# Performance work log

Measured on AMD Instinct MI355X. Metric: run time of the kernel, lower is better.

The kernel has to match this reference:

```python
import math
import jax, jax.numpy as jnp
import numpy as np

SAMPLE_RATIO = 0.25
K_NN = 5


def grid_index(loc_orig, H, W):
    # loc in [-1,1] -> nearest grid cell index (row-major)
    loc = jnp.clip(loc_orig, -1.0, 1.0) * 0.5 + 0.5
    ix = jnp.clip(jnp.round(loc[..., 0] * (W - 1)).astype(jnp.int32), 0, W - 1)
    iy = jnp.clip(jnp.round(loc[..., 1] * (H - 1)).astype(jnp.int32), 0, H - 1)
    return iy * W + ix  # [B, N0]


def token2map(x, loc_orig, idx_agg, H, W):
    # scatter token features (replicated to original points) into HxW grid, cell-average
    B, N, C = x.shape
    N0 = idx_agg.shape[1]
    idx_hw = grid_index(loc_orig, H, W)
    off = jnp.arange(B, dtype=jnp.int32)[:, None]
    idx_hw_flat = (idx_hw + off * (H * W)).reshape(-1)
    value = jnp.ones((B * N0,), x.dtype)
    all_w = jax.ops.segment_sum(value, idx_hw_flat, num_segments=B * H * W) + 1e-6
    value = value / all_w[idx_hw_flat]
    x_src = jnp.take_along_axis(x, idx_agg[..., None], axis=1).reshape(B * N0, C)
    x_map = jax.ops.segment_sum(x_src * value[:, None], idx_hw_flat, num_segments=B * H * W)
    return x_map.reshape(B, H, W, C).transpose(0, 3, 1, 2)  # [B,C,H,W]


def map2token(x_map, N, loc_orig, idx_agg, agg_weight):
    # gather grid features back to tokens, weighted by per-token-normalized agg_weight
    B, C, H, W = x_map.shape
    N0 = idx_agg.shape[1]
    idx_hw = grid_index(loc_orig, H, W)
    off = jnp.arange(B, dtype=jnp.int32)[:, None]
    idx_tok_flat = (idx_agg + off * N).reshape(-1)
    idx_hw_flat = (idx_hw + off * (H * W)).reshape(-1)
    value = agg_weight.reshape(-1).astype(x_map.dtype)
    all_w = jax.ops.segment_sum(value, idx_tok_flat, num_segments=B * N) + 1e-6
    value = value / all_w[idx_tok_flat]
    feat = x_map.transpose(0, 2, 3, 1).reshape(B * H * W, C)[idx_hw_flat]
    out = jax.ops.segment_sum(feat * value[:, None], idx_tok_flat, num_segments=B * N)
    return out.reshape(B, N, C)


def cluster_dpc_knn(x, Ns, k):
    # DPC-KNN clustering (no_grad in original -> stop_gradient)
    B, N, C = x.shape
    x = jax.lax.stop_gradient(x)
    x2 = jnp.sum(x * x, axis=-1)
    d2 = x2[:, :, None] + x2[:, None, :] - 2.0 * jnp.einsum('bic,bjc->bij', x, x)
    dist = jnp.sqrt(jnp.maximum(d2, 0.0)) / jnp.sqrt(jnp.asarray(C, x.dtype))
    dist_nearest = -jax.lax.top_k(-dist, k)[0]                 # k smallest dists (incl self)
    density = jnp.exp(-jnp.mean(dist_nearest ** 2, axis=-1))    # [B,N]
    # deterministic tiny tie-break noise (original uses torch.rand*1e-6)
    density = density + jax.random.uniform(jax.random.key(42), density.shape, density.dtype) * 1e-6
    mask = (density[:, None, :] > density[:, :, None]).astype(x.dtype)
    dist_max = jnp.max(dist.reshape(B, -1), axis=-1)[:, None, None]
    dist_ind = jnp.min(dist * mask + dist_max * (1.0 - mask), axis=-1)
    score = dist_ind * density
    index_down = jax.lax.top_k(score, Ns)[1]                    # [B,Ns] cluster centers
    dist_c = jnp.take_along_axis(dist, index_down[:, :, None], axis=1)  # [B,Ns,N]
    idx_cluster = jnp.argmin(dist_c, axis=1).astype(jnp.int32)  # [B,N]
    # centers belong to their own cluster
    flat = (index_down + jnp.arange(B)[:, None] * N).reshape(-1)
    own = jnp.tile(jnp.arange(Ns, dtype=jnp.int32), B)
    idx_cluster = idx_cluster.reshape(-1).at[flat].set(own).reshape(B, N)
    return idx_cluster


def merge_tokens(x, idx_cluster, Ns, weight, idx_agg):
    # weighted average of tokens per cluster; propagate mapping/weights to original points
    B, N, C = x.shape
    idx = (idx_cluster + jnp.arange(B, dtype=jnp.int32)[:, None] * Ns).reshape(-1)
    w = weight.reshape(-1)
    all_w = jax.ops.segment_sum(w, idx, num_segments=B * Ns) + 1e-6
    nw = w / all_w[idx]
    x_merged = jax.ops.segment_sum(x.reshape(B * N, C) * nw[:, None], idx,
                                   num_segments=B * Ns).reshape(B, Ns, C)
    norm_weight = nw.reshape(B, N, 1)
    idx_agg_new = jnp.take_along_axis(idx_cluster, idx_agg, axis=1)          # [B,N0]
    weight_t = jnp.take_along_axis(norm_weight, idx_agg[..., None], axis=1)  # [B,N0,1]
    return x_merged, idx_agg_new, weight_t


def ctm_forward(x, loc_orig, idx_agg, agg_weight, conv_w, conv_b, skip_w, ln_g, ln_b,
                conf_w, conf_b, H, W):
    B, N, C = x.shape
    x_map = token2map(x, loc_orig, idx_agg, H, W)
    x_map = jax.lax.conv_general_dilated(
        x_map, conv_w, window_strides=(2, 2), padding=((1, 1), (1, 1)),
        dimension_numbers=('NCHW', 'OIHW', 'NCHW')) + conv_b[None, :, None, None]
    xt = map2token(x_map, N, loc_orig, idx_agg, agg_weight) + x @ skip_w.T
    mu = jnp.mean(xt, axis=-1, keepdims=True)
    var = jnp.mean((xt - mu) ** 2, axis=-1, keepdims=True)
    xt = (xt - mu) / jnp.sqrt(var + 1e-5) * ln_g + ln_b
    conf = xt @ conf_w.T + conf_b          # [B,N,1]
    weight = jnp.exp(conf)
    Ns = max(math.ceil(N * SAMPLE_RATIO), 1)
    idx_cluster = cluster_dpc_knn(xt, Ns, K_NN)
    x_down, idx_agg_down, weight_t = merge_tokens(xt, idx_cluster, Ns, weight, idx_agg)
    agg_weight_down = agg_weight * weight_t
    agg_weight_down = agg_weight_down / jnp.max(agg_weight_down, axis=1, keepdims=True)
    # down_block is identity in this reference
    return x_down, idx_agg_down, agg_weight_down


def setup_inputs() -> dict:
    key = jax.random.key(0)
    ks = jax.random.split(key, 10)
    B, N, C, C2, H, W = 4, 3136, 64, 128, 56, 56
    return {
        'x': jax.random.normal(ks[0], (B, N, C), jnp.float32),
        'loc_orig': jax.random.normal(ks[1], (B, N, 2), jnp.float32),
        'idx_agg': jax.random.randint(ks[2], (B, N), 0, N),
        'agg_weight': jax.random.uniform(ks[3], (B, N, 1), jnp.float32, 0.1, 1.0),
        'conv_w': jax.random.normal(ks[4], (C2, C, 3, 3), jnp.float32) * 0.02,
        'conv_b': jnp.zeros((C2,), jnp.float32),
        'skip_w': jax.random.normal(ks[5], (C2, C), jnp.float32) * 0.02,
        'ln_g': jnp.ones((C2,), jnp.float32),
        'ln_b': jnp.zeros((C2,), jnp.float32),
        'conf_w': jax.random.normal(ks[6], (1, C2), jnp.float32) * 0.02,
        'conf_b': jnp.zeros((1,), jnp.float32),
        'H': 56,
        'W': 56,
    }


def reference(x, loc_orig, idx_agg, agg_weight, conv_w, conv_b, skip_w, ln_g, ln_b,
              conf_w, conf_b, H, W):
    return ctm_forward(x, loc_orig, idx_agg, agg_weight, conv_w, conv_b, skip_w,
                       ln_g, ln_b, conf_w, conf_b, H, W)
```

## Files before the change

### kernel.cpp

```cpp
#include <hip/hip_runtime.h>
#include <math.h>
#include <float.h>

#define Bq   4
#define Nq   3136
#define Cq   64
#define C2q  128
#define Hq   56
#define Wq   56
#define HWq  (Hq*Wq)
#define HOq  28
#define WOq  28
#define HWOq (HOq*WOq)
#define NSq  784
#define KNN  5
#define BNq  (Bq*Nq)

#define T64   64
#define KC    32
#define NIT64 (Nq/T64)
#define NT_C  ((NSq+T64-1)/T64)
#define NSPL  8
#define NSPA  2
#define LDP   34

__device__ __constant__ int c_spl[NSPL + 1]  = {0, 7, 13, 19, 25, 31, 37, 43, 49};
__device__ __constant__ int c_spla[NSPA + 1] = {0, 7, 13};

typedef unsigned int   u32;
typedef unsigned long long u64;
typedef __attribute__((ext_vector_type(4))) double d64x4;

static __device__ __forceinline__ void atomicMaxPosD(double* p, double v) {
    atomicMax((u64*)p, (u64)__double_as_longlong(v));
}
static __device__ __forceinline__ int clampTok(int t) {
    return min(max(t, 0), Nq - 1);
}

static __device__ __forceinline__ void ins5(double* a, double v) {
    if (v < a[KNN - 1]) {
        a[KNN - 1] = v;
        #pragma unroll
        for (int m = KNN - 1; m > 0; m--)
            if (a[m] < a[m - 1]) { double t = a[m]; a[m] = a[m - 1]; a[m - 1] = t; }
    }
}
static __device__ __forceinline__ void cex(double& a, double& b) {
    double lo = fmin(a, b), hi = fmax(a, b); a = lo; b = hi;
}
static __device__ __forceinline__ void merge5(double* a, const double* p) {
    double t0 = fmin(a[0], p[4]);
    double t1 = fmin(a[1], p[3]);
    double t2 = fmin(a[2], p[2]);
    double t3 = fmin(a[3], p[1]);
    double t4 = fmin(a[4], p[0]);
    cex(t0, t1); cex(t1, t2); cex(t2, t3); cex(t3, t4);
    cex(t0, t1); cex(t1, t2); cex(t2, t3);
    cex(t0, t1); cex(t1, t2);
    cex(t0, t1);
    a[0] = t0; a[1] = t1; a[2] = t2; a[3] = t3; a[4] = t4;
}

static __device__ __forceinline__ int mfma_mode_probe(int l4, int l15) {
    d64x4 p;
    #pragma unroll
    for (int v = 0; v < 4; v++) p[v] = 0.0;
    double a1 = (l4 == 0) ? (double)(16 * l15) : 0.0;
    double b1 = (l4 == 0) ? 1.0 : 0.0;
    p = __builtin_amdgcn_mfma_f64_16x16x4f64(a1, b1, p, 0, 0, 0);
    double a2 = (l4 == 0) ? 1.0 : 0.0;
    double b2 = (l4 == 0) ? (double)l15 : 0.0;
    p = __builtin_amdgcn_mfma_f64_16x16x4f64(a2, b2, p, 0, 0, 0);
    bool ok0 = true, ok1 = true;
    #pragma unroll
    for (int v = 0; v < 4; v++) {
        ok0 = ok0 && (p[v] == (double)(16 * (4 * l4 + v) + l15));
        ok1 = ok1 && (p[v] == (double)(16 * (l4 + 4 * v) + l15));
    }
    return __all(ok0) ? 0 : (__all(ok1) ? 1 : 2);
}

static __device__ __forceinline__ u32 rotl32(u32 x, int d) { return (x << d) | (x >> (32 - d)); }
static __device__ __forceinline__ float tf_uniform(int t) {
    const u32 k0 = 0u, k1 = 42u;
    const u32 ks2 = k0 ^ k1 ^ 0x1BD11BDAu;
    u32 ks[3] = { k0, k1, ks2 };
    bool lo = (t < 6272);
    u32 cx0 = lo ? (u32)t : (u32)(t - 6272);
    u32 cx1 = lo ? (u32)(t + 6272) : (u32)t;
    u32 x0 = cx0 + ks[0];
    u32 x1 = cx1 + ks[1];
    const int R0[4] = {13, 15, 26, 6};
    const int R1[4] = {17, 29, 16, 24};
    #pragma unroll
    for (int i = 0; i < 5; i++) {
        const int* rot = (i % 2 == 0) ? R0 : R1;
        #pragma unroll
        for (int r = 0; r < 4; r++) { x0 += x1; x1 = rotl32(x1, rot[r]); x1 ^= x0; }
        x0 += ks[(i + 1) % 3];
        x1 += ks[(i + 2) % 3] + (u32)(i + 1);
    }
    u32 bits = lo ? x0 : x1;
    u32 fb = (bits >> 9) | 0x3f800000u;
    float f; __builtin_memcpy(&f, &fb, 4);
    return f - 1.0f;
}

static __device__ __forceinline__ int gridIndex(float lx, float ly, int Wd, int Hd) {
    double x = fmin(fmax((double)lx, -1.0), 1.0) * 0.5 + 0.5;
    double y = fmin(fmax((double)ly, -1.0), 1.0) * 0.5 + 0.5;
    int ix = (int)rint(x * (double)(Wd - 1)); ix = min(max(ix, 0), Wd - 1);
    int iy = (int)rint(y * (double)(Hd - 1)); iy = min(max(iy, 0), Hd - 1);
    return iy * Wd + ix;
}

__global__ void ctm_fallback(float* out, int n) {
    int t = blockIdx.x * blockDim.x + threadIdx.x;
    if (t < n) out[t] = 0.0f;
}

__global__ void ctm_prep(const float* __restrict__ loc, const int* __restrict__ idx_agg,
                         const float* __restrict__ aggw,
                         int* cell56, int* cell28, int* cnt56, double* allwtok) {
    int t = blockIdx.x * blockDim.x + threadIdx.x;
    if (t >= BNq) return;
    int b = t / Nq;
    float lx = loc[2 * t], ly = loc[2 * t + 1];
    int c56 = gridIndex(lx, ly, Wq, Hq);
    int c28 = gridIndex(lx, ly, WOq, HOq);
    cell56[t] = c56; cell28[t] = c28;
    atomicAdd(&cnt56[b * HWq + c56], 1);
    int tok = clampTok(idx_agg[t]);
    atomicAdd(&allwtok[b * Nq + tok], (double)aggw[t]);
}

__global__ void ctm_t2m(const float* __restrict__ x, const int* __restrict__ idx_agg,
                        const int* __restrict__ cell56, const int* __restrict__ cnt56,
                        double* xmap56T) {
    int id = blockIdx.x * blockDim.x + threadIdx.x;
    if (id >= BNq * Cq) return;
    int t = id / Cq, c = id - t * Cq;
    int b = t / Nq;
    int cell = cell56[t];
    double v = 1.0 / ((double)cnt56[b * HWq + cell] + 1e-6);
    double xv = (double)x[(size_t)(b * Nq + clampTok(idx_agg[t])) * Cq + c];
    atomicAdd(&xmap56T[((size_t)b * HWq + cell) * Cq + c], xv * v);
}

__global__ void ctm_wt(const float* __restrict__ w, float* wT) {
    int id = blockIdx.x * blockDim.x + threadIdx.x;
    if (id >= C2q * Cq * 9) return;
    int co = id & (C2q - 1);
    int rem = id >> 7;
    int tap = rem % 9;
    int ci = rem / 9;
    wT[id] = w[(size_t)co * Cq * 9 + ci * 9 + tap];
}

__global__ __launch_bounds__(256)
void ctm_conv(const double* __restrict__ xmap56T, const float* __restrict__ wT,
              const float* __restrict__ bias, double* xmap28T) {
    __shared__ double sIn[2][9][Cq];
    int blk = blockIdx.x;
    int b  = blk & (Bq - 1);
    int cp = blk >> 2;
    int tid = threadIdx.x;
    int co = tid & (C2q - 1);
    int cl = tid >> 7;
    const double* xb = xmap56T + (size_t)b * HWq * Cq;
    for (int idx = tid; idx < 2 * 9 * Cq; idx += 256) {
        int cell_l = idx / (9 * Cq);
        int rem = idx - cell_l * (9 * Cq);
        int tap = rem >> 6;
        int ci  = rem & 63;
        int cell = 2 * cp + cell_l;
        int ox = cell % WOq, oy = cell / WOq;
        int ky = tap / 3, kx = tap - ky * 3;
        int iy = 2 * oy + ky - 1, ix = 2 * ox + kx - 1;
        double v = 0.0;
        if (iy >= 0 && iy < Hq && ix >= 0 && ix < Wq)
            v = xb[(size_t)(iy * Wq + ix) * Cq + ci];
        sIn[cell_l][tap][ci] = v;
    }
    __syncthreads();
    double acc = (double)bias[co];
    for (int ci = 0; ci < Cq; ci++) {
        #pragma unroll
        for (int tap = 0; tap < 9; tap++)
            acc += sIn[cl][tap][ci] * (double)wT[(size_t)(ci * 9 + tap) * C2q + co];
    }
    int cell = 2 * cp + cl;
    xmap28T[((size_t)b * HWOq + cell) * C2q + co] = acc;
}

__global__ void ctm_m2t(const double* __restrict__ xmap28T, const float* __restrict__ aggw,
                        const int* __restrict__ idx_agg, const int* __restrict__ cell28,
                        const double* __restrict__ allwtok, double* xt) {
    int id = blockIdx.x * blockDim.x + threadIdx.x;
    if (id >= BNq * C2q) return;
    int t = id / C2q, c = id - t * C2q;
    int b = t / Nq;
    int tok = clampTok(idx_agg[t]);
    double v = (double)aggw[t] / (allwtok[b * Nq + tok] + 1e-6);
    double f = xmap28T[((size_t)b * HWOq + cell28[t]) * C2q + c];
    atomicAdd(&xt[(size_t)(b * Nq + tok) * C2q + c], f * v);
}

__global__ __launch_bounds__(C2q)
void ctm_finalize(double* xt, const float* __restrict__ x, const float* __restrict__ skipw,
                  const float* __restrict__ lng, const float* __restrict__ lnb,
                  const float* __restrict__ confw, const float* __restrict__ confb,
                  double* x2o, double* weightv) {
    int bn = blockIdx.x; int c = threadIdx.x;
    int lane = c & 63, w = c >> 6;
    double* row = xt + (size_t)bn * C2q;
    const float* xr = x + (size_t)bn * Cq;
    double acc = row[c];
    const float* sw = skipw + c * Cq;
    #pragma unroll 16
    for (int k = 0; k < Cq; k++) acc += (double)xr[k] * (double)sw[k];
    __shared__ double slot[4][2];
    double s = acc;
    #pragma unroll
    for (int m = 1; m <= 32; m <<= 1) s += __shfl_xor(s, m);
    if (lane == 0) slot[0][w] = s;
    __syncthreads();
    double mu = (slot[0][0] + slot[0][1]) * (1.0 / C2q);
    double d = acc - mu;
    s = d * d;
    #pragma unroll
    for (int m = 1; m <= 32; m <<= 1) s += __shfl_xor(s, m);
    if (lane == 0) slot[1][w] = s;
    __syncthreads();
    double var = (slot[1][0] + slot[1][1]) * (1.0 / C2q);
    double v = d / sqrt(var + 1e-5) * (double)lng[c] + (double)lnb[c];
    row[c] = v;
    s = v * v;
    #pragma unroll
    for (int m = 1; m <= 32; m <<= 1) s += __shfl_xor(s, m);
    if (lane == 0) slot[2][w] = s;
    double s2 = v * (double)confw[c];
    #pragma unroll
    for (int m = 1; m <= 32; m <<= 1) s2 += __shfl_xor(s2, m);
    if (lane == 0) slot[3][w] = s2;
    __syncthreads();
    if (c == 0) {
        x2o[bn] = slot[2][0] + slot[2][1];
        weightv[bn] = exp(slot[3][0] + slot[3][1] + (double)confb[0]);
    }
}


__global__ __launch_bounds__(256, 2)
void ctm_pass1(const double* __restrict__ xt, const double* __restrict__ x2,
               double* pbest, double* pmax, double* d2buf, int dostore) {
    __shared__ double sBB[2][T64][LDP];
    __shared__ double sx2j[2][T64];
    int blk = blockIdx.x;
    int b  = blk & (Bq - 1);
    int s  = (blk >> 2) & (NSPL - 1);
    int it = blk >> 5;
    int tid = threadIdx.x;
    const double* xtb = xt + (size_t)b * Nq * C2q;
    const double* x2b = x2 + (size_t)b * Nq;
    int i0 = it * T64;
    int jt_beg = c_spl[s], jt_end = c_spl[s + 1];

    int wv = tid >> 6, ln = tid & 63;
    int l15 = ln & 15, l4 = ln >> 4;
    int mode = mfma_mode_probe(l4, l15);

    if (mode < 2) {
        int rw[4];
        #pragma unroll
        for (int v = 0; v < 4; v++) rw[v] = (mode == 0) ? (4 * l4 + v) : (l4 + 4 * v);
        int rbase = i0 + wv * 16;
        double a_reg[4][8];
        const double* arow = xtb + (size_t)(i0 + wv * 16 + l15) * C2q + l4;
        #pragma unroll
        for (int kc = 0; kc < 4; kc++)
            #pragma unroll
            for (int st = 0; st < 8; st++)
                a_reg[kc][st] = arow[kc * KC + 4 * st];
        double x2i[4];
        #pragma unroll
        for (int v = 0; v < 4; v++) x2i[v] = x2b[rbase + rw[v]];
        double best[4][KNN]; double mx[4];
        #pragma unroll
        for (int v = 0; v < 4; v++) {
            mx[v] = -DBL_MAX;
            #pragma unroll
            for (int k = 0; k < KNN; k++) best[v][k] = DBL_MAX;
        }
        {
            int j0 = jt_beg * T64;
            #pragma unroll
            for (int w = 0; w < 4; w++) {
                int idx = tid + w * 256; int r = idx >> 4, c = (idx & 15) * 2;
                *(double2*)&sBB[0][r][c] = *(const double2*)&xtb[(size_t)(j0 + r) * C2q + c];
            }
            if (tid < T64) sx2j[0][tid] = x2b[j0 + tid];
        }
        __syncthreads();
        int q = 0;
        for (int jt = jt_beg; jt < jt_end; jt++) {
            int j0 = jt * T64;
            d64x4 acc[4];
            #pragma unroll
            for (int bc = 0; bc < 4; bc++)
                #pragma unroll
                for (int v = 0; v < 4; v++) acc[bc][v] = 0.0;
            #pragma unroll
            for (int kc = 0; kc < 4; kc++) {
                const int cb = kc & 1, nb = cb ^ 1, nkc = (kc + 1) & 3;
                const bool lastk = (kc == 3);
                bool hn = !lastk || (jt + 1 < jt_end);
                int nj0 = lastk ? j0 + T64 : j0;
                double2 sreg[4]; double xr = 0.0;
                if (hn) {
                    #pragma unroll
                    for (int w = 0; w < 4; w++) {
                        int idx = tid + w * 256; int r = idx >> 4, c = (idx & 15) * 2;
                        sreg[w] = *(const double2*)&xtb[(size_t)(nj0 + r) * C2q + nkc * KC + c];
                    }
                    if (lastk && tid < T64) xr = x2b[nj0 + tid];
                }
                #pragma unroll
                for (int st = 0; st < 8; st++) {
                    double av = a_reg[kc][st];
                    #pragma unroll
                    for (int bc = 0; bc < 4; bc++) {
                        double bv = sBB[cb][bc * 16 + l15][4 * st + l4];
                        acc[bc] = __builtin_amdgcn_mfma_f64_16x16x4f64(av, bv, acc[bc], 0, 0, 0);
                    }
                }
                if (hn) {
                    #pragma unroll
                    for (int w = 0; w < 4; w++) {
                        int idx = tid + w * 256; int r = idx >> 4, c = (idx & 15) * 2;
                        *(double2*)&sBB[nb][r][c] = sreg[w];
                    }
                    if (lastk && tid < T64) sx2j[q ^ 1][tid] = xr;
                }
                __syncthreads();
            }
            #pragma unroll
            for (int bc = 0; bc < 4; bc++) {
                double xj = sx2j[q][bc * 16 + l15];
                #pragma unroll
                for (int v = 0; v < 4; v++) {
                    double d2 = x2i[v] + xj - 2.0 * acc[bc][v];
                    if (dostore)
                        d2buf[(size_t)(b * Nq + rbase + rw[v]) * Nq + (j0 + bc * 16 + l15)] = d2;
                    mx[v] = fmax(mx[v], d2);
                    ins5(best[v], d2);
                }
            }
            q ^= 1;
        }
        for (int m = 1; m <= 8; m <<= 1) {
            #pragma unroll
            for (int v = 0; v < 4; v++) {
                double p[KNN];
                #pragma unroll
                for (int k = 0; k < KNN; k++) p[k] = __shfl_xor(best[v][k], m);
                mx[v] = fmax(mx[v], __shfl_xor(mx[v], m));
                merge5(best[v], p);
            }
        }
        if (l15 == 0) {
            #pragma unroll
            for (int v = 0; v < 4; v++) {
                int gi = b * Nq + rbase + rw[v];
                size_t base = ((size_t)s * BNq + gi) * KNN;
                #pragma unroll
                for (int k = 0; k < KNN; k++) pbest[base + k] = best[v][k];
                pmax[(size_t)s * BNq + gi] = mx[v];
            }
        }
    } else {
        double (*sA)[LDP] = sBB[0];
        double (*sB)[LDP] = sBB[1];
        int tx = tid & 15, ty = tid >> 4;
        double x2i[4];
        #pragma unroll
        for (int r = 0; r < 4; r++) x2i[r] = x2b[i0 + ty + 16 * r];
        double best[4][KNN]; double mx[4];
        #pragma unroll
        for (int r = 0; r < 4; r++) {
            mx[r] = -DBL_MAX;
            #pragma unroll
            for (int k = 0; k < KNN; k++) best[r][k] = DBL_MAX;
        }
        for (int jt = jt_beg; jt < jt_end; jt++) {
            int j0 = jt * T64;
            double acc[4][4];
            #pragma unroll
            for (int r = 0; r < 4; r++)
                #pragma unroll
                for (int q = 0; q < 4; q++) acc[r][q] = 0.0;
            for (int kc = 0; kc < 4; kc++) {
                __syncthreads();
                #pragma unroll
                for (int idx = tid; idx < T64 * KC / 2; idx += 256) {
                    int r = idx >> 4, c = (idx & 15) * 2;
                    *(double2*)&sA[r][c] = *(const double2*)&xtb[(size_t)(i0 + r) * C2q + kc * KC + c];
                    *(double2*)&sB[r][c] = *(const double2*)&xtb[(size_t)(j0 + r) * C2q + kc * KC + c];
                }
                if (kc == 0 && tid < T64) sx2j[0][tid] = x2b[j0 + tid];
                __syncthreads();
                #pragma unroll 4
                for (int cc = 0; cc < KC; cc += 2) {
                    double2 xi[4], xj[4];
                    #pragma unroll
                    for (int r = 0; r < 4; r++) xi[r] = *(const double2*)&sA[ty + 16 * r][cc];
                    #pragma unroll
                    for (int q = 0; q < 4; q++) xj[q] = *(const double2*)&sB[tx + 16 * q][cc];
                    #pragma unroll
                    for (int r = 0; r < 4; r++)
                        #pragma unroll
                        for (int q = 0; q < 4; q++) acc[r][q] += xi[r].x * xj[q].x;
                    #pragma unroll
                    for (int r = 0; r < 4; r++)
                        #pragma unroll
                        for (int q = 0; q < 4; q++) acc[r][q] += xi[r].y * xj[q].y;
                }
            }
            #pragma unroll
            for (int r = 0; r < 4; r++)
                #pragma unroll
                for (int q = 0; q < 4; q++) {
                    double d2 = x2i[r] + sx2j[0][tx + 16 * q] - 2.0 * acc[r][q];
                    if (dostore)
                        d2buf[(size_t)(b * Nq + i0 + ty + 16 * r) * Nq + (j0 + tx + 16 * q)] = d2;
                    mx[r] = fmax(mx[r], d2);
                    ins5(best[r], d2);
                }
        }
        for (int m = 1; m <= 8; m <<= 1) {
            #pragma unroll
            for (int r = 0; r < 4; r++) {
                double p[KNN];
                #pragma unroll
                for (int k = 0; k < KNN; k++) p[k] = __shfl_xor(best[r][k], m);
                mx[r] = fmax(mx[r], __shfl_xor(mx[r], m));
                merge5(best[r], p);
            }
        }
        if (tx == 0) {
            #pragma unroll
            for (int r = 0; r < 4; r++) {
                int gi = b * Nq + i0 + ty + 16 * r;
                size_t base = ((size_t)s * BNq + gi) * KNN;
                #pragma unroll
                for (int k = 0; k < KNN; k++) pbest[base + k] = best[r][k];
                pmax[(size_t)s * BNq + gi] = mx[r];
            }
        }
    }
}

__global__ void ctm_merge1(const double* __restrict__ pbest, const double* __restrict__ pmax,
                           double* density, double* maxd2) {
    int t = blockIdx.x * blockDim.x + threadIdx.x;
    if (t >= BNq) return;
    double a[KNN];
    #pragma unroll
    for (int k = 0; k < KNN; k++) a[k] = pbest[(size_t)t * KNN + k];
    double mxv = pmax[t];
    #pragma unroll
    for (int s = 1; s < NSPL; s++) {
        double p[KNN];
        #pragma unroll
        for (int k = 0; k < KNN; k++) p[k] = pbest[((size_t)s * BNq + t) * KNN + k];
        merge5(a, p);
        mxv = fmax(mxv, pmax[(size_t)s * BNq + t]);
    }
    double sum = 0.0;
    #pragma unroll
    for (int k = 0; k < KNN; k++) sum += fmax(a[k], 0.0);
    density[t] = exp(-sum / (double)(C2q * KNN)) + (double)(tf_uniform(t) * 1e-6f);
    atomicMaxPosD(&maxd2[t / Nq], mxv);
}

__global__ __launch_bounds__(256)
void ctm_pass2s(const double* __restrict__ d2buf, const double* __restrict__ density,
                double* pmin2) {
    int gid = blockIdx.x * 4 + (threadIdx.x >> 6);
    int lane = threadIdx.x & 63;
    if (gid >= BNq) return;
    int b = gid / Nq;
    int i = gid - b * Nq;
    const double* dr = d2buf + (size_t)gid * Nq;
    const double* db = density + (size_t)b * Nq;
    double di = db[i];
    double mn = DBL_MAX;
    for (int j = lane; j < Nq; j += 64) {
        double d2 = dr[j];
        if (db[j] > di) mn = fmin(mn, d2);
    }
    #pragma unroll
    for (int m = 1; m <= 32; m <<= 1) mn = fmin(mn, __shfl_xor(mn, m));
    if (lane == 0) pmin2[gid] = mn;
}

__global__ void ctm_merge2s(const double* __restrict__ pmin2, const double* __restrict__ maxd2,
                            const double* __restrict__ density, double* score) {
    int t = blockIdx.x * blockDim.x + threadIdx.x;
    if (t >= BNq) return;
    int b = t / Nq;
    double mm = fmin(maxd2[b], pmin2[t]);
    score[t] = sqrt(fmax(mm, 0.0)) / sqrt((double)C2q) * density[t];
}

__global__ __launch_bounds__(256, 2)
void ctm_pass2(const double* __restrict__ xt, const double* __restrict__ x2,
               const double* __restrict__ density, double* pmin) {
    __shared__ double sBB[2][T64][LDP];
    __shared__ double sx2j[2][T64];
    __shared__ double sdj[2][T64];
    int blk = blockIdx.x;
    int b  = blk & (Bq - 1);
    int s  = (blk >> 2) & (NSPL - 1);
    int it = blk >> 5;
    int tid = threadIdx.x;
    const double* xtb = xt + (size_t)b * Nq * C2q;
    const double* x2b = x2 + (size_t)b * Nq;
    const double* db  = density + (size_t)b * Nq;
    int i0 = it * T64;
    int jt_beg = c_spl[s], jt_end = c_spl[s + 1];

    int wv = tid >> 6, ln = tid & 63;
    int l15 = ln & 15, l4 = ln >> 4;
    int mode = mfma_mode_probe(l4, l15);

    if (mode < 2) {
        int rw[4];
        #pragma unroll
        for (int v = 0; v < 4; v++) rw[v] = (mode == 0) ? (4 * l4 + v) : (l4 + 4 * v);
        int rbase = i0 + wv * 16;
        double a_reg[4][8];
        const double* arow = xtb + (size_t)(i0 + wv * 16 + l15) * C2q + l4;
        #pragma unroll
        for (int kc = 0; kc < 4; kc++)
            #pragma unroll
            for (int st = 0; st < 8; st++)
                a_reg[kc][st] = arow[kc * KC + 4 * st];
        double x2i[4], di[4], mn[4];
        #pragma unroll
        for (int v = 0; v < 4; v++) {
            x2i[v] = x2b[rbase + rw[v]];
            di[v]  = db[rbase + rw[v]];
            mn[v]  = DBL_MAX;
        }
        {
            int j0 = jt_beg * T64;
            #pragma unroll
            for (int w = 0; w < 4; w++) {
                int idx = tid + w * 256; int r = idx >> 4, c = (idx & 15) * 2;
                *(double2*)&sBB[0][r][c] = *(const double2*)&xtb[(size_t)(j0 + r) * C2q + c];
            }
            if (tid < T64) { sx2j[0][tid] = x2b[j0 + tid]; sdj[0][tid] = db[j0 + tid]; }
        }
        __syncthreads();
        int q = 0;
        for (int jt = jt_beg; jt < jt_end; jt++) {
            int j0 = jt * T64;
            d64x4 acc[4];
            #pragma unroll
            for (int bc = 0; bc < 4; bc++)
                #pragma unroll
                for (int v = 0; v < 4; v++) acc[bc][v] = 0.0;
            #pragma unroll
            for (int kc = 0; kc < 4; kc++) {
                const int cb = kc & 1, nb = cb ^ 1, nkc = (kc + 1) & 3;
                const bool lastk = (kc == 3);
                bool hn = !lastk || (jt + 1 < jt_end);
                int nj0 = lastk ? j0 + T64 : j0;
                double2 sreg[4]; double xr = 0.0, dr = 0.0;
                if (hn) {
                    #pragma unroll
                    for (int w = 0; w < 4; w++) {
                        int idx = tid + w * 256; int r = idx >> 4, c = (idx & 15) * 2;
                        sreg[w] = *(const double2*)&xtb[(size_t)(nj0 + r) * C2q + nkc * KC + c];
                    }
                    if (lastk && tid < T64) { xr = x2b[nj0 + tid]; dr = db[nj0 + tid]; }
                }
                #pragma unroll
                for (int st = 0; st < 8; st++) {
                    double av = a_reg[kc][st];
                    #pragma unroll
                    for (int bc = 0; bc < 4; bc++) {
                        double bv = sBB[cb][bc * 16 + l15][4 * st + l4];
                        acc[bc] = __builtin_amdgcn_mfma_f64_16x16x4f64(av, bv, acc[bc], 0, 0, 0);
                    }
                }
                if (hn) {
                    #pragma unroll
                    for (int w = 0; w < 4; w++) {
                        int idx = tid + w * 256; int r = idx >> 4, c = (idx & 15) * 2;
                        *(double2*)&sBB[nb][r][c] = sreg[w];
                    }
                    if (lastk && tid < T64) { sx2j[q ^ 1][tid] = xr; sdj[q ^ 1][tid] = dr; }
                }
                __syncthreads();
            }
            #pragma unroll
            for (int bc = 0; bc < 4; bc++) {
                double xj = sx2j[q][bc * 16 + l15];
                double dj = sdj[q][bc * 16 + l15];
                #pragma unroll
                for (int v = 0; v < 4; v++) {
                    double d2 = x2i[v] + xj - 2.0 * acc[bc][v];
                    if (dj > di[v]) mn[v] = fmin(mn[v], d2);
                }
            }
            q ^= 1;
        }
        for (int m = 1; m <= 8; m <<= 1) {
            #pragma unroll
            for (int v = 0; v < 4; v++) mn[v] = fmin(mn[v], __shfl_xor(mn[v], m));
        }
        if (l15 == 0) {
            #pragma unroll
            for (int v = 0; v < 4; v++) {
                int gi = b * Nq + rbase + rw[v];
                pmin[(size_t)s * BNq + gi] = mn[v];
            }
        }
    } else {
        double (*sA)[LDP] = sBB[0];
        double (*sB)[LDP] = sBB[1];
        int tx = tid & 15, ty = tid >> 4;
        double x2i[4], di[4], mn[4];
        #pragma unroll
        for (int r = 0; r < 4; r++) {
            x2i[r] = x2b[i0 + ty + 16 * r];
            di[r]  = db[i0 + ty + 16 * r];
            mn[r]  = DBL_MAX;
        }
        for (int jt = jt_beg; jt < jt_end; jt++) {
            int j0 = jt * T64;
            double acc[4][4];
            #pragma unroll
            for (int r = 0; r < 4; r++)
                #pragma unroll
                for (int q = 0; q < 4; q++) acc[r][q] = 0.0;
            for (int kc = 0; kc < 4; kc++) {
                __syncthreads();
                #pragma unroll
                for (int idx = tid; idx < T64 * KC / 2; idx += 256) {
                    int r = idx >> 4, c = (idx & 15) * 2;
                    *(double2*)&sA[r][c] = *(const double2*)&xtb[(size_t)(i0 + r) * C2q + kc * KC + c];
                    *(double2*)&sB[r][c] = *(const double2*)&xtb[(size_t)(j0 + r) * C2q + kc * KC + c];
                }
                if (kc == 0 && tid < T64) { sx2j[0][tid] = x2b[j0 + tid]; sdj[0][tid] = db[j0 + tid]; }
                __syncthreads();
                #pragma unroll 4
                for (int cc = 0; cc < KC; cc += 2) {
                    double2 xi[4], xj[4];
                    #pragma unroll
                    for (int r = 0; r < 4; r++) xi[r] = *(const double2*)&sA[ty + 16 * r][cc];
                    #pragma unroll
                    for (int q = 0; q < 4; q++) xj[q] = *(const double2*)&sB[tx + 16 * q][cc];
                    #pragma unroll
                    for (int r = 0; r < 4; r++)
                        #pragma unroll
                        for (int q = 0; q < 4; q++) acc[r][q] += xi[r].x * xj[q].x;
                    #pragma unroll
                    for (int r = 0; r < 4; r++)
                        #pragma unroll
                        for (int q = 0; q < 4; q++) acc[r][q] += xi[r].y * xj[q].y;
                }
            }
            #pragma unroll
            for (int r = 0; r < 4; r++)
                #pragma unroll
                for (int q = 0; q < 4; q++) {
                    double d2 = x2i[r] + sx2j[0][tx + 16 * q] - 2.0 * acc[r][q];
                    if (sdj[0][tx + 16 * q] > di[r]) mn[r] = fmin(mn[r], d2);
                }
        }
        for (int m = 1; m <= 8; m <<= 1) {
            #pragma unroll
            for (int r = 0; r < 4; r++) mn[r] = fmin(mn[r], __shfl_xor(mn[r], m));
        }
        if (tx == 0) {
            #pragma unroll
            for (int r = 0; r < 4; r++) {
                int gi = b * Nq + i0 + ty + 16 * r;
                pmin[(size_t)s * BNq + gi] = mn[r];
            }
        }
    }
}

__global__ void ctm_merge2(const double* __restrict__ pmin, const double* __restrict__ maxd2,
                           const double* __restrict__ density, double* score) {
    int t = blockIdx.x * blockDim.x + threadIdx.x;
    if (t >= BNq) return;
    int b = t / Nq;
    double m = pmin[t];
    #pragma unroll
    for (int s = 1; s < NSPL; s++) m = fmin(m, pmin[(size_t)s * BNq + t]);
    double mm = fmin(maxd2[b], m);
    score[t] = sqrt(fmax(mm, 0.0)) / sqrt((double)C2q) * density[t];
}

__global__ __launch_bounds__(1024)
void ctm_sort(const double* __restrict__ score, int* index_down) {
    __shared__ double s[4096];
    __shared__ int   si[4096];
    int b = blockIdx.x, tid = threadIdx.x;
    for (int i = tid; i < 4096; i += 1024) {
        if (i < Nq) {
            double v = score[b * Nq + i];
            s[i] = isnan(v) ? -DBL_MAX : v;
            si[i] = i;
        } else { s[i] = -DBL_MAX; si[i] = 0x7fffffff; }
    }
    __syncthreads();
    for (int k = 2; k <= 4096; k <<= 1) {
        for (int j = k >> 1; j > 0; j >>= 1) {
            for (int i = tid; i < 4096; i += 1024) {
                int ixj = i ^ j;
                if (ixj > i) {
                    double s1 = s[i], s2 = s[ixj];
                    int i1 = si[i], i2 = si[ixj];
                    bool before_ij = (s1 > s2) || (s1 == s2 && i1 < i2);
                    bool before_ji = (s2 > s1) || (s2 == s1 && i2 < i1);
                    bool doswap = ((i & k) == 0) ? before_ji : before_ij;
                    if (doswap) { s[i] = s2; s[ixj] = s1; si[i] = i2; si[ixj] = i1; }
                }
            }
            __syncthreads();
        }
    }
    for (int t = tid; t < NSq; t += 1024) {
        int v = si[t];
        index_down[b * NSq + t] = ((unsigned)v < (unsigned)Nq) ? v : 0;
    }
}

__global__ __launch_bounds__(256, 2)
void ctm_assign(const double* __restrict__ xt, const double* __restrict__ x2,
                const int* __restrict__ index_down, double* pbd, int* pbs) {
    __shared__ double sBB[2][T64][LDP];
    __shared__ double sx2c[T64];
    __shared__ int    sidx[T64];
    int blk = blockIdx.x;
    int b  = blk & (Bq - 1);
    int s  = (blk >> 2) & (NSPA - 1);
    int it = blk >> 3;
    int tid = threadIdx.x;
    const double* xtb = xt + (size_t)b * Nq * C2q;
    const double* x2b = x2 + (size_t)b * Nq;
    int i0 = it * T64;
    int jt_beg = c_spla[s], jt_end = c_spla[s + 1];

    int wv = tid >> 6, ln = tid & 63;
    int l15 = ln & 15, l4 = ln >> 4;
    int mode = mfma_mode_probe(l4, l15);

    if (mode < 2) {
        int rw[4];
        #pragma unroll
        for (int v = 0; v < 4; v++) rw[v] = (mode == 0) ? (4 * l4 + v) : (l4 + 4 * v);
        int rbase = i0 + wv * 16;
        double a_reg[4][8];
        const double* arow = xtb + (size_t)(i0 + wv * 16 + l15) * C2q + l4;
        #pragma unroll
        for (int kc = 0; kc < 4; kc++)
            #pragma unroll
            for (int st = 0; st < 8; st++)
                a_reg[kc][st] = arow[kc * KC + 4 * st];
        double x2i[4], bd[4];
        int bs[4];
        #pragma unroll
        for (int v = 0; v < 4; v++) { x2i[v] = x2b[rbase + rw[v]]; bd[v] = DBL_MAX; bs[v] = NSq - 1; }
        for (int jt = jt_beg; jt < jt_end; jt++) {
            int j0 = jt * T64;
            __syncthreads();
            if (tid < T64) {
                int j = index_down[b * NSq + min(j0 + tid, NSq - 1)];
                sidx[tid] = j;
                sx2c[tid] = x2b[j];
            }
            __syncthreads();
            d64x4 acc[4];
            #pragma unroll
            for (int bc = 0; bc < 4; bc++)
                #pragma unroll
                for (int v = 0; v < 4; v++) acc[bc][v] = 0.0;
            for (int kc = 0; kc < 4; kc++) {
                if (kc) __syncthreads();
                #pragma unroll
                for (int idx = tid; idx < T64 * KC / 2; idx += 256) {
                    int r = idx >> 4, c = (idx & 15) * 2;
                    *(double2*)&sBB[0][r][c] = *(const double2*)&xtb[(size_t)sidx[r] * C2q + kc * KC + c];
                }
                __syncthreads();
                #pragma unroll
                for (int st = 0; st < 8; st++) {
                    double av = a_reg[kc][st];
                    #pragma unroll
                    for (int bc = 0; bc < 4; bc++) {
                        double bv = sBB[0][bc * 16 + l15][4 * st + l4];
                        acc[bc] = __builtin_amdgcn_mfma_f64_16x16x4f64(av, bv, acc[bc], 0, 0, 0);
                    }
                }
            }
            #pragma unroll
            for (int bc = 0; bc < 4; bc++) {
                int sc = j0 + bc * 16 + l15;
                double xc = sx2c[bc * 16 + l15];
                #pragma unroll
                for (int v = 0; v < 4; v++) {
                    double d = fmax(x2i[v] + xc - 2.0 * acc[bc][v], 0.0);
                    if (sc < NSq && (d < bd[v] || (d == bd[v] && sc < bs[v]))) { bd[v] = d; bs[v] = sc; }
                }
            }
        }
        for (int m = 1; m <= 8; m <<= 1) {
            #pragma unroll
            for (int v = 0; v < 4; v++) {
                double pd = __shfl_xor(bd[v], m);
                int    ps = __shfl_xor(bs[v], m);
                if (pd < bd[v] || (pd == bd[v] && ps < bs[v])) { bd[v] = pd; bs[v] = ps; }
            }
        }
        if (l15 == 0) {
            #pragma unroll
            for (int v = 0; v < 4; v++) {
                int gi = b * Nq + rbase + rw[v];
                pbd[(size_t)s * BNq + gi] = bd[v];
                pbs[(size_t)s * BNq + gi] = bs[v];
            }
        }
    } else {
        double (*sA)[LDP] = sBB[0];
        double (*sB)[LDP] = sBB[1];
        int tx = tid & 15, ty = tid >> 4;
        double x2i[4], bd[4];
        int bs[4];
        #pragma unroll
        for (int r = 0; r < 4; r++) { x2i[r] = x2b[i0 + ty + 16 * r]; bd[r] = DBL_MAX; bs[r] = NSq - 1; }
        for (int jt = jt_beg; jt < jt_end; jt++) {
            int j0 = jt * T64;
            __syncthreads();
            if (tid < T64) {
                int j = index_down[b * NSq + min(j0 + tid, NSq - 1)];
                sidx[tid] = j;
                sx2c[tid] = x2b[j];
            }
            __syncthreads();
            double acc[4][4];
            #pragma unroll
            for (int r = 0; r < 4; r++)
                #pragma unroll
                for (int q = 0; q < 4; q++) acc[r][q] = 0.0;
            for (int kc = 0; kc < 4; kc++) {
                if (kc) __syncthreads();
                #pragma unroll
                for (int idx = tid; idx < T64 * KC / 2; idx += 256) {
                    int r = idx >> 4, c = (idx & 15) * 2;
                    *(double2*)&sA[r][c] = *(const double2*)&xtb[(size_t)(i0 + r) * C2q + kc * KC + c];
                    *(double2*)&sB[r][c] = *(const double2*)&xtb[(size_t)sidx[r] * C2q + kc * KC + c];
                }
                __syncthreads();
                #pragma unroll 4
                for (int cc = 0; cc < KC; cc += 2) {
                    double2 xi[4], xj[4];
                    #pragma unroll
                    for (int r = 0; r < 4; r++) xi[r] = *(const double2*)&sA[ty + 16 * r][cc];
                    #pragma unroll
                    for (int q = 0; q < 4; q++) xj[q] = *(const double2*)&sB[tx + 16 * q][cc];
                    #pragma unroll
                    for (int r = 0; r < 4; r++)
                        #pragma unroll
                        for (int q = 0; q < 4; q++) acc[r][q] += xi[r].x * xj[q].x;
                    #pragma unroll
                    for (int r = 0; r < 4; r++)
                        #pragma unroll
                        for (int q = 0; q < 4; q++) acc[r][q] += xi[r].y * xj[q].y;
                }
            }
            #pragma unroll
            for (int r = 0; r < 4; r++)
                #pragma unroll
                for (int q = 0; q < 4; q++) {
                    int sc = j0 + tx + 16 * q;
                    double d = fmax(x2i[r] + sx2c[tx + 16 * q] - 2.0 * acc[r][q], 0.0);
                    if (sc < NSq && (d < bd[r] || (d == bd[r] && sc < bs[r]))) { bd[r] = d; bs[r] = sc; }
                }
        }
        for (int m = 1; m <= 8; m <<= 1) {
            #pragma unroll
            for (int r = 0; r < 4; r++) {
                double pd = __shfl_xor(bd[r], m);
                int    ps = __shfl_xor(bs[r], m);
                if (pd < bd[r] || (pd == bd[r] && ps < bs[r])) { bd[r] = pd; bs[r] = ps; }
            }
        }
        if (tx == 0) {
            #pragma unroll
            for (int r = 0; r < 4; r++) {
                int gi = b * Nq + i0 + ty + 16 * r;
                pbd[(size_t)s * BNq + gi] = bd[r];
                pbs[(size_t)s * BNq + gi] = bs[r];
            }
        }
    }
}

__global__ void ctm_merge3(const double* __restrict__ pbd, const int* __restrict__ pbs,
                           int* idx_cluster) {
    int t = blockIdx.x * blockDim.x + threadIdx.x;
    if (t >= BNq) return;
    double d0 = pbd[t];          int s0 = pbs[t];
    double d1 = pbd[BNq + t];    int s1 = pbs[BNq + t];
    bool take1 = (d1 < d0) || (d1 == d0 && s1 < s0);
    idx_cluster[t] = take1 ? s1 : s0;
}

__global__ void ctm_override(const int* __restrict__ index_down, int* idx_cluster) {
    int t = blockIdx.x * blockDim.x + threadIdx.x;
    if (t >= Bq * NSq) return;
    int b = t / NSq, sc = t - b * NSq;
    int j = index_down[t];
    if ((unsigned)j < (unsigned)Nq) idx_cluster[b * Nq + j] = sc;
}

__global__ void ctm_zeromerged(double* xmerged) {
    int t = blockIdx.x * blockDim.x + threadIdx.x;
    if (t < Bq * NSq * C2q) xmerged[t] = 0.0;
}

__global__ void ctm_merge_w(const int* __restrict__ idx_cluster, const double* __restrict__ weightv,
                            double* allwc) {
    int t = blockIdx.x * blockDim.x + threadIdx.x;
    if (t >= BNq) return;
    int b = t / Nq;
    int sc = min(max(idx_cluster[t], 0), NSq - 1);
    atomicAdd(&allwc[b * NSq + sc], weightv[t]);
}

__global__ void ctm_merge_x(const int* __restrict__ idx_cluster, const double* __restrict__ weightv,
                            const double* __restrict__ allwc, const double* __restrict__ xt,
                            double* nw, double* xmerged) {
    int id = blockIdx.x * blockDim.x + threadIdx.x;
    if (id >= BNq * C2q) return;
    int t = id / C2q, c = id - t * C2q;
    int b = t / Nq;
    int sc = min(max(idx_cluster[t], 0), NSq - 1);
    double nv = weightv[t] / (allwc[b * NSq + sc] + 1e-6);
    if (c == 0) nw[t] = nv;
    atomicAdd(&xmerged[((size_t)(b * NSq + sc)) * C2q + c], xt[(size_t)t * C2q + c] * nv);
}

__global__ void ctm_out0(const double* __restrict__ xmerged, float* out) {
    int t = blockIdx.x * blockDim.x + threadIdx.x;
    if (t >= Bq * NSq * C2q) return;
    out[t] = (float)xmerged[t];
}

__global__ void ctm_out12(const int* __restrict__ idx_agg, const int* __restrict__ idx_cluster,
                          const double* __restrict__ nw, const float* __restrict__ aggw,
                          float* out1, double* awd, double* maxawd) {
    int t = blockIdx.x * blockDim.x + threadIdx.x;
    if (t >= BNq) return;
    int b = t / Nq;
    int tok = clampTok(idx_agg[t]);
    int sc = idx_cluster[b * Nq + tok];
    out1[t] = (float)sc;
    double a = (double)aggw[t] * nw[b * Nq + tok];
    awd[t] = a;
    atomicMaxPosD(&maxawd[b], a);
}

__global__ void ctm_out2(const double* __restrict__ awd, const double* __restrict__ maxawd, float* out2) {
    int t = blockIdx.x * blockDim.x + threadIdx.x;
    if (t >= BNq) return;
    int b = t / Nq;
    out2[t] = (float)(awd[t] / maxawd[b]);
}

extern "C" void kernel_launch(void* const* d_in, const int* in_sizes, int n_in,
                              void* d_out, int out_size, void* d_ws, size_t ws_size,
                              hipStream_t stream) {
    const float* x     = (const float*)d_in[0];
    const float* loc   = (const float*)d_in[1];
    const int*   idxag = (const int*)  d_in[2];
    const float* aggw  = (const float*)d_in[3];
    const float* convw = (const float*)d_in[4];
    const float* convb = (const float*)d_in[5];
    const float* skipw = (const float*)d_in[6];
    const float* lng   = (const float*)d_in[7];
    const float* lnb   = (const float*)d_in[8];
    const float* confw = (const float*)d_in[9];
    const float* confb = (const float*)d_in[10];
    (void)in_sizes; (void)n_in;

    char* w = (char*)d_ws;
    size_t off = 0;
    auto alloc = [&](size_t bytes) -> void* {
        void* p = w + off; off = (off + bytes + 255) & ~(size_t)255; return p;
    };

    int*    cnt56   = (int*)   alloc((size_t)BNq * 4);
    double* allwtok = (double*)alloc((size_t)BNq * 8);
    double* xt      = (double*)alloc((size_t)BNq * C2q * 8);
    double* arena   = (double*)alloc((size_t)Bq * HWq * Cq * 8);
    double* allwc   = (double*)alloc((size_t)Bq * NSq * 8);
    double* maxawd  = (double*)alloc((size_t)Bq * 8);
    double* maxd2   = (double*)alloc((size_t)Bq * 8);
    size_t zero_bytes = off;
    int*    cell56   = (int*)   alloc((size_t)BNq * 4);
    int*    cell28   = (int*)   alloc((size_t)BNq * 4);
    double* xmap28T  = (double*)alloc((size_t)Bq * HWOq * C2q * 8);
    float*  wT       = (float*) alloc((size_t)C2q * Cq * 9 * 4);
    double* x2       = (double*)alloc((size_t)BNq * 8);
    double* density  = (double*)alloc((size_t)BNq * 8);
    double* score    = (double*)alloc((size_t)BNq * 8);
    int*    indexdn  = (int*)   alloc((size_t)Bq * NSq * 4);
    int*    idxclu   = (int*)   alloc((size_t)BNq * 4);
    double* nw       = (double*)alloc((size_t)BNq * 8);
    double* weightv  = (double*)alloc((size_t)BNq * 8);
    double* awd      = (double*)alloc((size_t)BNq * 8);
    double* pbest    = (double*)alloc((size_t)NSPL * BNq * KNN * 8);
    double* pmax     = (double*)alloc((size_t)NSPL * BNq * 8);
    double* pmin     = (double*)alloc((size_t)NSPL * BNq * 8);
    double* pbd      = (double*)alloc((size_t)NSPA * BNq * 8);
    int*    pbs      = (int*)   alloc((size_t)NSPA * BNq * 4);
    size_t required = off;
    double* d2buf    = (double*)alloc((size_t)BNq * Nq * 8);
    size_t required_fast = off;

    const int tb = 256;
    float* out = (float*)d_out;

    if (ws_size < required) {
        ctm_fallback<<<(out_size + tb - 1) / tb, tb, 0, stream>>>(out, out_size);
        return;
    }
    const bool fast = (ws_size >= required_fast);

    double* xmap56T = arena;
    double* xmerged = arena;

    hipMemsetAsync(d_ws, 0, zero_bytes, stream);

    ctm_prep<<<(BNq + tb - 1) / tb, tb, 0, stream>>>(loc, idxag, aggw, cell56, cell28, cnt56, allwtok);
    ctm_wt<<<((C2q * Cq * 9) + tb - 1) / tb, tb, 0, stream>>>(convw, wT);
    ctm_t2m<<<((BNq * Cq) + tb - 1) / tb, tb, 0, stream>>>(x, idxag, cell56, cnt56, xmap56T);
    ctm_conv<<<Bq * (HWOq / 2), 256, 0, stream>>>(xmap56T, wT, convb, xmap28T);
    ctm_m2t<<<((BNq * C2q) + tb - 1) / tb, tb, 0, stream>>>(xmap28T, aggw, idxag, cell28, allwtok, xt);
    ctm_finalize<<<BNq, C2q, 0, stream>>>(xt, x, skipw, lng, lnb, confw, confb, x2, weightv);
    ctm_pass1<<<Bq * NSPL * NIT64, 256, 0, stream>>>(xt, x2, pbest, pmax, d2buf, fast ? 1 : 0);
    ctm_merge1<<<(BNq + tb - 1) / tb, tb, 0, stream>>>(pbest, pmax, density, maxd2);
    if (fast) {
        ctm_pass2s<<<(BNq + 3) / 4, 256, 0, stream>>>(d2buf, density, pmin);
        ctm_merge2s<<<(BNq + tb - 1) / tb, tb, 0, stream>>>(pmin, maxd2, density, score);
    } else {
        ctm_pass2<<<Bq * NSPL * NIT64, 256, 0, stream>>>(xt, x2, density, pmin);
        ctm_merge2<<<(BNq + tb - 1) / tb, tb, 0, stream>>>(pmin, maxd2, density, score);
    }
    ctm_sort<<<Bq, 1024, 0, stream>>>(score, indexdn);
    ctm_assign<<<Bq * NSPA * NIT64, 256, 0, stream>>>(xt, x2, indexdn, pbd, pbs);
    ctm_merge3<<<(BNq + tb - 1) / tb, tb, 0, stream>>>(pbd, pbs, idxclu);
    ctm_override<<<((Bq * NSq) + tb - 1) / tb, tb, 0, stream>>>(indexdn, idxclu);
    ctm_zeromerged<<<((Bq * NSq * C2q) + tb - 1) / tb, tb, 0, stream>>>(xmerged);
    ctm_merge_w<<<(BNq + tb - 1) / tb, tb, 0, stream>>>(idxclu, weightv, allwc);
    ctm_merge_x<<<((BNq * C2q) + tb - 1) / tb, tb, 0, stream>>>(idxclu, weightv, allwc, xt, nw, xmerged);

    ctm_out0<<<((Bq * NSq * C2q) + tb - 1) / tb, tb, 0, stream>>>(xmerged, out);
    ctm_out12<<<(BNq + tb - 1) / tb, tb, 0, stream>>>(idxag, idxclu, nw, aggw,
                                                      out + (size_t)Bq * NSq * C2q, awd, maxawd);
    ctm_out2<<<(BNq + tb - 1) / tb, tb, 0, stream>>>(awd, maxawd,
                                                     out + (size_t)Bq * NSq * C2q + BNq);
}
```

Measured before the change: 1.237 ms.

## Replace stored distance matrix with density-sorted triangular recompute pass

Drops the full BxNxN fp64 distance buffer that pass1 wrote and pass2s re-read. Tokens are instead sorted by density, features are permuted, and a triangular MFMA pass recomputes distances only for pairs where the other token has higher density. Per-tile partial minima are then merged and scattered back to the original order. This cuts a large amount of HBM write and read traffic and about half the pass2 compute, at the cost of a bitonic sort, a permutation copy, and a change in tie-handling semantics for equal densities.

Result: no change. 1.249 ms (+0.9%).

```diff
diff --git a/kernel.cpp b/kernel.cpp
--- a/kernel.cpp
+++ b/kernel.cpp
@@ -19,7 +19,7 @@
 #define T64   64
 #define KC    32
 #define NIT64 (Nq/T64)
-#define NT_C  ((NSq+T64-1)/T64)
+#define NPAIR (NIT64*(NIT64+1)/2)
 #define NSPL  8
 #define NSPA  2
 #define LDP   34
@@ -254,7 +254,7 @@
 
 __global__ __launch_bounds__(256, 2)
 void ctm_pass1(const double* __restrict__ xt, const double* __restrict__ x2,
-               double* pbest, double* pmax, double* d2buf, int dostore) {
+               double* pbest, double* pmax) {
     __shared__ double sBB[2][T64][LDP];
     __shared__ double sx2j[2][T64];
     int blk = blockIdx.x;
@@ -351,8 +351,6 @@
                 #pragma unroll
                 for (int v = 0; v < 4; v++) {
                     double d2 = x2i[v] + xj - 2.0 * acc[bc][v];
-                    if (dostore)
-                        d2buf[(size_t)(b * Nq + rbase + rw[v]) * Nq + (j0 + bc * 16 + l15)] = d2;
                     mx[v] = fmax(mx[v], d2);
                     ins5(best[v], d2);
                 }
@@ -432,8 +430,6 @@
                 #pragma unroll
                 for (int q = 0; q < 4; q++) {
                     double d2 = x2i[r] + sx2j[0][tx + 16 * q] - 2.0 * acc[r][q];
-                    if (dostore)
-                        d2buf[(size_t)(b * Nq + i0 + ty + 16 * r) * Nq + (j0 + tx + 16 * q)] = d2;
                     mx[r] = fmax(mx[r], d2);
                     ins5(best[r], d2);
                 }
@@ -484,34 +480,192 @@
     atomicMaxPosD(&maxd2[t / Nq], mxv);
 }
 
-__global__ __launch_bounds__(256)
-void ctm_pass2s(const double* __restrict__ d2buf, const double* __restrict__ density,
-                double* pmin2) {
-    int gid = blockIdx.x * 4 + (threadIdx.x >> 6);
-    int lane = threadIdx.x & 63;
-    if (gid >= BNq) return;
-    int b = gid / Nq;
-    int i = gid - b * Nq;
-    const double* dr = d2buf + (size_t)gid * Nq;
-    const double* db = density + (size_t)b * Nq;
-    double di = db[i];
-    double mn = DBL_MAX;
-    for (int j = lane; j < Nq; j += 64) {
-        double d2 = dr[j];
-        if (db[j] > di) mn = fmin(mn, d2);
-    }
-    #pragma unroll
-    for (int m = 1; m <= 32; m <<= 1) mn = fmin(mn, __shfl_xor(mn, m));
-    if (lane == 0) pmin2[gid] = mn;
-}
-
-__global__ void ctm_merge2s(const double* __restrict__ pmin2, const double* __restrict__ maxd2,
-                            const double* __restrict__ density, double* score) {
+__global__ __launch_bounds__(1024)
+void ctm_sortd(const double* __restrict__ density, int* perm) {
+    __shared__ double s[4096];
+    __shared__ int   si[4096];
+    int b = blockIdx.x, tid = threadIdx.x;
+    for (int i = tid; i < 4096; i += 1024) {
+        if (i < Nq) {
+            double v = density[b * Nq + i];
+            s[i] = isnan(v) ? -DBL_MAX : v;
+            si[i] = i;
+        } else { s[i] = -DBL_MAX; si[i] = 0x7fffffff; }
+    }
+    __syncthreads();
+    for (int k = 2; k <= 4096; k <<= 1) {
+        for (int j = k >> 1; j > 0; j >>= 1) {
+            for (int i = tid; i < 4096; i += 1024) {
+                int ixj = i ^ j;
+                if (ixj > i) {
+                    double s1 = s[i], s2 = s[ixj];
+                    int i1 = si[i], i2 = si[ixj];
+                    bool before_ij = (s1 > s2) || (s1 == s2 && i1 < i2);
+                    bool before_ji = (s2 > s1) || (s2 == s1 && i2 < i1);
+                    bool doswap = ((i & k) == 0) ? before_ji : before_ij;
+                    if (doswap) { s[i] = s2; s[ixj] = s1; si[i] = i2; si[ixj] = i1; }
+                }
+            }
+            __syncthreads();
+        }
+    }
+    for (int t = tid; t < Nq; t += 1024) {
+        int v = si[t];
+        perm[b * Nq + t] = ((unsigned)v < (unsigned)Nq) ? v : 0;
+    }
+}
+
+__global__ void ctm_perm(const double* __restrict__ xt, const double* __restrict__ x2,
+                         const int* __restrict__ perm, double* xtp, double* x2p) {
+    int id = blockIdx.x * blockDim.x + threadIdx.x;
+    if (id >= BNq * C2q) return;
+    int t = id / C2q, c = id - t * C2q;
+    int b = t / Nq;
+    int p = perm[t];
+    int src = b * Nq + p;
+    xtp[(size_t)t * C2q + c] = xt[(size_t)src * C2q + c];
+    if (c == 0) x2p[t] = x2[src];
+}
+
+__global__ __launch_bounds__(256, 2)
+void ctm_pass2t(const double* __restrict__ xtp, const double* __restrict__ x2p,
+                double* pminP) {
+    __shared__ double sBB[2][T64][LDP];
+    __shared__ double sx2j[T64];
+    __shared__ double sp[4][T64];
+    int blk = blockIdx.x;
+    int b = blk & (Bq - 1);
+    int p = blk >> 2;
+    int it = (int)((sqrt(8.0 * (double)p + 1.0) - 1.0) * 0.5);
+    while ((it + 1) * (it + 2) / 2 <= p) ++it;
+    while (it * (it + 1) / 2 > p) --it;
+    int jt = p - it * (it + 1) / 2;
+    int i0 = it * T64, j0 = jt * T64;
+    int tid = threadIdx.x;
+    const double* xb  = xtp + (size_t)b * Nq * C2q;
+    const double* x2b = x2p + (size_t)b * Nq;
+    int wv = tid >> 6, ln = tid & 63;
+    int l15 = ln & 15, l4 = ln >> 4;
+    int mode = mfma_mode_probe(l4, l15);
+
+    if (mode < 2) {
+        int rw[4];
+        #pragma unroll
+        for (int v = 0; v < 4; v++) rw[v] = (mode == 0) ? (4 * l4 + v) : (l4 + 4 * v);
+        int rbase = i0 + wv * 16;
+        double a_reg[4][8];
+        const double* arow = xb + (size_t)(rbase + l15) * C2q + l4;
+        #pragma unroll
+        for (int kc = 0; kc < 4; kc++)
+            #pragma unroll
+            for (int st = 0; st < 8; st++)
+                a_reg[kc][st] = arow[kc * KC + 4 * st];
+        double x2i[4];
+        #pragma unroll
+        for (int v = 0; v < 4; v++) x2i[v] = x2b[rbase + rw[v]];
+        #pragma unroll
+        for (int w = 0; w < 4; w++) {
+            int idx = tid + w * 256; int r = idx >> 4, c = (idx & 15) * 2;
+            *(double2*)&sBB[0][r][c] = *(const double2*)&xb[(size_t)(j0 + r) * C2q + c];
+        }
+        if (tid < T64) sx2j[tid] = x2b[j0 + tid];
+        __syncthreads();
+        d64x4 acc[4];
+        #pragma unroll
+        for (int bc = 0; bc < 4; bc++)
+            #pragma unroll
+            for (int v = 0; v < 4; v++) acc[bc][v] = 0.0;
+        #pragma unroll
+        for (int kc = 0; kc < 4; kc++) {
+            const int cb = kc & 1, nb = cb ^ 1;
+            const bool hn = (kc < 3);
+            double2 sreg[4];
+            if (hn) {
+                #pragma unroll
+                for (int w = 0; w < 4; w++) {
+                    int idx = tid + w * 256; int r = idx >> 4, c = (idx & 15) * 2;
+                    sreg[w] = *(const double2*)&xb[(size_t)(j0 + r) * C2q + (kc + 1) * KC + c];
+                }
+            }
+            #pragma unroll
+            for (int st = 0; st < 8; st++) {
+                double av = a_reg[kc][st];
+                #pragma unroll
+                for (int bc = 0; bc < 4; bc++) {
+                    double bv = sBB[cb][bc * 16 + l15][4 * st + l4];
+                    acc[bc] = __builtin_amdgcn_mfma_f64_16x16x4f64(av, bv, acc[bc], 0, 0, 0);
+                }
+            }
+            if (hn) {
+                #pragma unroll
+                for (int w = 0; w < 4; w++) {
+                    int idx = tid + w * 256; int r = idx >> 4, c = (idx & 15) * 2;
+                    *(double2*)&sBB[nb][r][c] = sreg[w];
+                }
+            }
+            __syncthreads();
+        }
+        double mn[4];
+        #pragma unroll
+        for (int v = 0; v < 4; v++) mn[v] = DBL_MAX;
+        #pragma unroll
+        for (int bc = 0; bc < 4; bc++) {
+            int cg = j0 + bc * 16 + l15;
+            double xj = sx2j[bc * 16 + l15];
+            #pragma unroll
+            for (int v = 0; v < 4; v++) {
+                double d2 = x2i[v] + xj - 2.0 * acc[bc][v];
+                bool valid = (jt < it) || (cg < rbase + rw[v]);
+                if (valid) mn[v] = fmin(mn[v], d2);
+            }
+        }
+        for (int m = 1; m <= 8; m <<= 1) {
+            #pragma unroll
+            for (int v = 0; v < 4; v++) mn[v] = fmin(mn[v], __shfl_xor(mn[v], m));
+        }
+        if (l15 == 0) {
+            #pragma unroll
+            for (int v = 0; v < 4; v++)
+                pminP[(size_t)jt * BNq + b * Nq + rbase + rw[v]] = mn[v];
+        }
+    } else {
+        int rl = tid & 63;
+        int cg4 = tid >> 6;
+        int r = i0 + rl;
+        double x2i = x2b[r];
+        const double* xr = xb + (size_t)r * C2q;
+        double mn = DBL_MAX;
+        for (int cc = 0; cc < 16; cc++) {
+            int cglob = j0 + cg4 * 16 + cc;
+            if (jt == it && cglob >= r) continue;
+            const double* xc = xb + (size_t)cglob * C2q;
+            double dot = 0.0;
+            for (int k = 0; k < C2q; k++) dot += xr[k] * xc[k];
+            double d2 = x2i + x2b[cglob] - 2.0 * dot;
+            mn = fmin(mn, d2);
+        }
+        sp[cg4][rl] = mn;
+        __syncthreads();
+        if (cg4 == 0) {
+            mn = fmin(fmin(sp[0][rl], sp[1][rl]), fmin(sp[2][rl], sp[3][rl]));
+            pminP[(size_t)jt * BNq + b * Nq + r] = mn;
+        }
+    }
+}
+
+__global__ void ctm_merge2t(const double* __restrict__ pminP, const double* __restrict__ maxd2,
+                            const double* __restrict__ density, const int* __restrict__ perm,
+                            double* score) {
     int t = blockIdx.x * blockDim.x + threadIdx.x;
     if (t >= BNq) return;
     int b = t / Nq;
-    double mm = fmin(maxd2[b], pmin2[t]);
-    score[t] = sqrt(fmax(mm, 0.0)) / sqrt((double)C2q) * density[t];
+    int rr = t - b * Nq;
+    int it = rr >> 6;
+    double m = DBL_MAX;
+    for (int jt = 0; jt <= it; jt++) m = fmin(m, pminP[(size_t)jt * BNq + t]);
+    double mm = fmin(maxd2[b], m);
+    int orig = b * Nq + perm[t];
+    score[orig] = sqrt(fmax(mm, 0.0)) / sqrt((double)C2q) * density[orig];
 }
 
 __global__ __launch_bounds__(256, 2)
@@ -1034,8 +1188,11 @@
     double* pbd      = (double*)alloc((size_t)NSPA * BNq * 8);
     int*    pbs      = (int*)   alloc((size_t)NSPA * BNq * 4);
     size_t required = off;
-    double* d2buf    = (double*)alloc((size_t)BNq * Nq * 8);
-    size_t required_fast = off;
+    int*    perm     = (int*)   alloc((size_t)BNq * 4);
+    double* x2p      = (double*)alloc((size_t)BNq * 8);
+    double* xtp      = (double*)alloc((size_t)BNq * C2q * 8);
+    double* pminP    = (double*)alloc((size_t)NIT64 * BNq * 8);
+    size_t required_tri = off;
 
     const int tb = 256;
     float* out = (float*)d_out;
@@ -1044,7 +1201,7 @@
         ctm_fallback<<<(out_size + tb - 1) / tb, tb, 0, stream>>>(out, out_size);
         return;
     }
-    const bool fast = (ws_size >= required_fast);
+    const bool tri = (ws_size >= required_tri);
 
     double* xmap56T = arena;
     double* xmerged = arena;
@@ -1057,11 +1214,13 @@
     ctm_conv<<<Bq * (HWOq / 2), 256, 0, stream>>>(xmap56T, wT, convb, xmap28T);
     ctm_m2t<<<((BNq * C2q) + tb - 1) / tb, tb, 0, stream>>>(xmap28T, aggw, idxag, cell28, allwtok, xt);
     ctm_finalize<<<BNq, C2q, 0, stream>>>(xt, x, skipw, lng, lnb, confw, confb, x2, weightv);
-    ctm_pass1<<<Bq * NSPL * NIT64, 256, 0, stream>>>(xt, x2, pbest, pmax, d2buf, fast ? 1 : 0);
+    ctm_pass1<<<Bq * NSPL * NIT64, 256, 0, stream>>>(xt, x2, pbest, pmax);
     ctm_merge1<<<(BNq + tb - 1) / tb, tb, 0, stream>>>(pbest, pmax, density, maxd2);
-    if (fast) {
-        ctm_pass2s<<<(BNq + 3) / 4, 256, 0, stream>>>(d2buf, density, pmin);
-        ctm_merge2s<<<(BNq + tb - 1) / tb, tb, 0, stream>>>(pmin, maxd2, density, score);
+    if (tri) {
+        ctm_sortd<<<Bq, 1024, 0, stream>>>(density, perm);
+        ctm_perm<<<((BNq * C2q) + tb - 1) / tb, tb, 0, stream>>>(xt, x2, perm, xtp, x2p);
+        ctm_pass2t<<<Bq * NPAIR, 256, 0, stream>>>(xtp, x2p, pminP);
+        ctm_merge2t<<<(BNq + tb - 1) / tb, tb, 0, stream>>>(pminP, maxd2, density, perm, score);
     } else {
         ctm_pass2<<<Bq * NSPL * NIT64, 256, 0, stream>>>(xt, x2, density, pmin);
         ctm_merge2<<<(BNq + tb - 1) / tb, tb, 0, stream>>>(pmin, maxd2, density, score);
```
